# Optimization experiments

Measured on AMD Instinct MI355X. Metric: run time of the kernel, lower is better.

Reference implementation:

```python
import jax, jax.numpy as jnp
import numpy as np

B, N, CIN = 4, 8192, 256
H, D = 8, 64            # n_heads, head_n_channels
INNER = H * D           # 512
COUT = 256
EPS = 1e-5              # torch InstanceNorm1d default eps


def setup_inputs() -> dict:
    key = jax.random.key(0)
    ks = jax.random.split(key, 8)
    s = 1.0 / np.sqrt(CIN)
    return {
        "u_x": jax.random.normal(ks[0], (B, N, CIN), dtype=jnp.float32),
        "pos_x": jax.random.uniform(ks[1], (B, N, 2), dtype=jnp.float32),
        # torch nn.Linear weights have shape (out_features, in_features)
        "Wq": jax.random.normal(ks[2], (INNER, CIN), dtype=jnp.float32) * s,
        "Wk": jax.random.normal(ks[3], (INNER, CIN), dtype=jnp.float32) * s,
        "Wv": jax.random.normal(ks[4], (INNER, CIN), dtype=jnp.float32) * s,
        "Wo": jax.random.normal(ks[5], (COUT, INNER), dtype=jnp.float32) * (1.0 / np.sqrt(INNER)),
        "bo": jax.random.normal(ks[6], (COUT,), dtype=jnp.float32) * 0.01,
    }


def _heads(x, W):
    # x: [B,N,CIN] @ W.T -> [B,N,H*D] -> [B,H,N,D]
    y = jnp.einsum("bnc,ec->bne", x, W)
    return y.reshape(x.shape[0], x.shape[1], H, D).transpose(0, 2, 1, 3)


def _inorm(u):
    # Matches torch: InstanceNorm1d applied to (B*H, N, D) normalizes over the
    # LAST dim (D) per (batch, head, grid point), biased variance, no affine.
    mean = jnp.mean(u, axis=-1, keepdims=True)
    var = jnp.mean(jnp.square(u - mean), axis=-1, keepdims=True)
    return (u - mean) / jnp.sqrt(var + EPS)


def reference(u_x, pos_x, Wq, Wk, Wv, Wo, bo):
    batch, n = u_x.shape[0], u_x.shape[1]
    q = _heads(u_x, Wq)          # [B,H,N,D]
    k = _inorm(_heads(u_x, Wk))  # u_y = u_x (self-attention path)
    v = _inorm(_heads(u_x, Wv))
    # associative path: (K^T V) then Q; uniform weights = 1/N
    dots = jnp.einsum("bhnd,bhne->bhde", k, v)   # [B,H,D,D]
    u = jnp.einsum("bhnd,bhde->bhne", q, dots) / n
    u = u.transpose(0, 2, 1, 3).reshape(batch, n, INNER)
    return jnp.einsum("bne,oe->bno", u, Wo) + bo
```

## Files before the change

kernel.cpp:

```cpp
#include <hip/hip_runtime.h>


#define B_    4
#define N_    8192
#define CIN_  256
#define H_    8
#define D_    64
#define INNER_ 512
#define COUT_ 256
#define EPS_  1e-5f

typedef unsigned short ushort_t;
typedef unsigned int   uint_t;
typedef __attribute__((ext_vector_type(8))) short short8;
typedef __attribute__((ext_vector_type(4))) float f32x4;

__device__ __forceinline__ void split_bf16(float x, ushort_t& hi, ushort_t& lo) {
  const uint_t u = __float_as_uint(x);
  const uint_t hr = (u + 0x8000u) & 0xffff0000u;
  hi = (ushort_t)(hr >> 16);
  const float l = x - __uint_as_float(hr);
  lo = (ushort_t)((__float_as_uint(l) + 0x8000u) >> 16);
}

__device__ __forceinline__ void cvt8(float4 x, float4 y, uint4& uh, uint4& ul) {
  const float v[8] = {x.x, x.y, x.z, x.w, y.x, y.y, y.z, y.w};
  ushort_t h[8], l[8];
#pragma unroll
  for (int j = 0; j < 8; j++) split_bf16(v[j], h[j], l[j]);
  uh = make_uint4(h[0] | ((uint_t)h[1] << 16), h[2] | ((uint_t)h[3] << 16),
                  h[4] | ((uint_t)h[5] << 16), h[6] | ((uint_t)h[7] << 16));
  ul = make_uint4(l[0] | ((uint_t)l[1] << 16), l[2] | ((uint_t)l[3] << 16),
                  l[4] | ((uint_t)l[5] << 16), l[6] | ((uint_t)l[7] << 16));
}

#define MFMA(A, Bv, C) __builtin_amdgcn_mfma_f32_16x16x32_bf16((A), (Bv), (C), 0, 0, 0)


__global__ __launch_bounds__(256) void prep_ux_kernel(
    const float* __restrict__ u_x, ushort_t* __restrict__ uxH,
    ushort_t* __restrict__ uxL)
{
  const int w = threadIdx.x >> 6, lane = threadIdx.x & 63;
  const uint_t tile = blockIdx.x * 4 + w;
  const uint_t kt = tile & 7, ntg = tile >> 3;
  const uint_t r = lane & 15, qv = lane >> 4;
  const size_t src = ((size_t)ntg * 16 + r) * 256 + kt * 32 + qv * 8;
  const float4 x = *(const float4*)(u_x + src);
  const float4 y = *(const float4*)(u_x + src + 4);
  uint4 uh, ul;
  cvt8(x, y, uh, ul);
  const size_t dst = (size_t)tile * 512 + (size_t)lane * 8;
  *(uint4*)(uxH + dst) = uh;
  *(uint4*)(uxL + dst) = ul;
}

__global__ __launch_bounds__(256) void prep_w_kernel(
    const float* __restrict__ Wk, const float* __restrict__ Wv,
    ushort_t* __restrict__ WkvH, ushort_t* __restrict__ WkvL)
{
  const uint_t tid = blockIdx.x * 256 + threadIdx.x;
  const uint_t rr = tid >> 5;
  const uint_t c0 = (tid & 31) * 8;
  const float* src = (rr < 512) ? (Wk + (size_t)rr * CIN_ + c0)
                                : (Wv + (size_t)(rr - 512) * CIN_ + c0);
  const float4 x = *(const float4*)(src);
  const float4 y = *(const float4*)(src + 4);
  uint4 uh, ul;
  cvt8(x, y, uh, ul);
  const uint_t kt = c0 >> 5, qq = (c0 >> 3) & 3;
  const uint_t lanei = (rr & 15) | (qq << 4);
  const size_t dst = (((size_t)(rr >> 4) * 8 + kt) * 64 + lanei) * 8;
  *(uint4*)(WkvH + dst) = uh;
  *(uint4*)(WkvL + dst) = ul;
}

__global__ __launch_bounds__(256, 2) void kv_dots_kernel(
    const ushort_t* __restrict__ uxH, const ushort_t* __restrict__ uxL,
    const ushort_t* __restrict__ WkvH, const ushort_t* __restrict__ WkvL,
    float* __restrict__ dots)
{
  __shared__ __align__(16) char smem[32768];
  ushort_t* KtH = (ushort_t*)(smem);
  ushort_t* KtL = (ushort_t*)(smem + 8192);
  ushort_t* VtH = (ushort_t*)(smem + 16384);
  ushort_t* VtL = (ushort_t*)(smem + 24576);

  const int t = threadIdx.x;
  const int chunk = blockIdx.x, h = blockIdx.y, b = blockIdx.z;
  const int lane = t & 63, wave = t >> 6;
  const int q = lane >> 4, r = lane & 15;
  const int m0 = (wave >> 1) * 64;
  const int dstripe = 16 * wave;
  const size_t laneoff = (size_t)lane * 8;

  const int rtB0 = ((wave & 1) ? 32 : 0) + h * 4;

  f32x4 dacc[4];
#pragma unroll
  for (int j = 0; j < 4; j++) dacc[j] = (f32x4)0.f;

  for (int mt = 0; mt < 2; mt++) {
    const int nt0 = chunk * 16 + mt * 8 + (m0 >> 4);

    f32x4 acc[4][4];
#pragma unroll
    for (int i = 0; i < 4; i++)
#pragma unroll
      for (int j = 0; j < 4; j++) acc[i][j] = (f32x4)0.f;

    for (int kc = 0; kc < 8; kc++) {
      short8 ahf[4], alf[4];
#pragma unroll
      for (int mi = 0; mi < 4; mi++) {
        const size_t toff =
            (((size_t)b * 512 + nt0 + mi) * 8 + kc) * 512 + laneoff;
        ahf[mi] = *(const short8*)(uxH + toff);
        alf[mi] = *(const short8*)(uxL + toff);
      }
#pragma unroll
      for (int nj = 0; nj < 4; nj++) {
        const size_t boff = ((size_t)(rtB0 + nj) * 8 + kc) * 512 + laneoff;
        const short8 bhv = *(const short8*)(WkvH + boff);
        const short8 blv = *(const short8*)(WkvL + boff);
#pragma unroll
        for (int mi = 0; mi < 4; mi++) {
          acc[mi][nj] = MFMA(ahf[mi], bhv, acc[mi][nj]);
          acc[mi][nj] = MFMA(alf[mi], bhv, acc[mi][nj]);
          acc[mi][nj] = MFMA(ahf[mi], blv, acc[mi][nj]);
        }
      }
    }

    float mean[4][4], inv[4][4];
#pragma unroll
    for (int mi = 0; mi < 4; mi++)
#pragma unroll
      for (int reg = 0; reg < 4; reg++) {
        float rs = 0.f, rq = 0.f;
#pragma unroll
        for (int nj = 0; nj < 4; nj++) {
          const float v = acc[mi][nj][reg];
          rs += v;
          rq = fmaf(v, v, rq);
        }
#pragma unroll
        for (int msk = 1; msk < 16; msk <<= 1) {
          rs += __shfl_xor(rs, msk, 64);
          rq += __shfl_xor(rq, msk, 64);
        }
        const float m = rs * (1.f / 64.f);
        const float var = fmaxf(rq * (1.f / 64.f) - m * m, 0.f);
        mean[mi][reg] = m;
        inv[mi][reg] = rsqrtf(var + EPS_);
      }
#pragma unroll
    for (int mi = 0; mi < 4; mi++)
#pragma unroll
      for (int nj = 0; nj < 4; nj++)
#pragma unroll
        for (int reg = 0; reg < 4; reg++)
          acc[mi][nj][reg] = (acc[mi][nj][reg] - mean[mi][reg]) * inv[mi][reg];

    for (int p = 0; p < 2; p++) {
      if ((wave >> 1) == p) {
        ushort_t* Hd = (wave & 1) ? VtH : KtH;
        ushort_t* Ld = (wave & 1) ? VtL : KtL;
#pragma unroll
        for (int nj = 0; nj < 4; nj++) {
          const int d = 16 * nj + r;
#pragma unroll
          for (int mi = 0; mi < 4; mi++) {
            ushort_t hh[4], ll[4];
#pragma unroll
            for (int reg = 0; reg < 4; reg++)
              split_bf16(acc[mi][nj][reg], hh[reg], ll[reg]);
            uint2 ph, pl;
            ph.x = hh[0] | ((uint_t)hh[1] << 16);
            ph.y = hh[2] | ((uint_t)hh[3] << 16);
            pl.x = ll[0] | ((uint_t)ll[1] << 16);
            pl.y = ll[2] | ((uint_t)ll[3] << 16);
            const int bw = ((4 * mi + q) ^ ((d & 7) << 1)) * 4;
            *(uint2*)&Hd[d * 64 + bw] = ph;
            *(uint2*)&Ld[d * 64 + bw] = pl;
          }
        }
      }
      __syncthreads();
#pragma unroll
      for (int ks = 0; ks < 2; ks++) {
        const int ra = dstripe + r;
        const int ca = ((ks * 4 + q) ^ (ra & 7)) * 8;
        const short8 aH = *(const short8*)&KtH[ra * 64 + ca];
        const short8 aL = *(const short8*)&KtL[ra * 64 + ca];
#pragma unroll
        for (int ej = 0; ej < 4; ej++) {
          const int rb = 16 * ej + r;
          const int cb = ((ks * 4 + q) ^ (rb & 7)) * 8;
          const short8 bH = *(const short8*)&VtH[rb * 64 + cb];
          const short8 bL = *(const short8*)&VtL[rb * 64 + cb];
          dacc[ej] = MFMA(aH, bH, dacc[ej]);
          dacc[ej] = MFMA(aL, bH, dacc[ej]);
          dacc[ej] = MFMA(aH, bL, dacc[ej]);
        }
      }
      __syncthreads();
    }
  }

  float* dg = dots + ((size_t)(b * H_ + h)) * 4096;
#pragma unroll
  for (int ej = 0; ej < 4; ej++)
#pragma unroll
    for (int reg = 0; reg < 4; reg++)
      atomicAdd(&dg[(dstripe + 4 * q + reg) * 64 + 16 * ej + r], dacc[ej][reg]);
}

__global__ __launch_bounds__(256) void s_kernel(
    const float* __restrict__ dots, const float* __restrict__ Wo,
    float* __restrict__ S)
{
  const int blk = blockIdx.x;
  const int b = blk >> 9, hd = blk & 511, h = hd >> 6;
  __shared__ float drow[64];
  const int t = threadIdx.x;
  if (t < 64) drow[t] = dots[((size_t)(b * H_ + h)) * 4096 + (hd & 63) * 64 + t];
  __syncthreads();
  const float* wp = Wo + (size_t)t * INNER_ + h * 64;
  float acc = 0.f;
#pragma unroll
  for (int e = 0; e < 64; e += 4) {
    const float4 w = *(const float4*)(wp + e);
    acc = fmaf(drow[e + 0], w.x, acc);
    acc = fmaf(drow[e + 1], w.y, acc);
    acc = fmaf(drow[e + 2], w.z, acc);
    acc = fmaf(drow[e + 3], w.w, acc);
  }
  S[((size_t)(b * INNER_) + hd) * COUT_ + t] = acc;
}

__global__ __launch_bounds__(256) void mb_part_kernel(
    const float* __restrict__ Wq, const float* __restrict__ S,
    float* __restrict__ Mbp)
{
  __shared__ __align__(16) float wql[128][16];
  const int c0 = blockIdx.x * 16, b = blockIdx.y, s = blockIdx.z;
  const int t = threadIdx.x;
#pragma unroll
  for (int i = 0; i < 8; i++) {
    const int idx = i * 256 + t;
    wql[idx >> 4][idx & 15] = Wq[(size_t)(s * 128 + (idx >> 4)) * CIN_ + c0 + (idx & 15)];
  }
  __syncthreads();
  float acc[16];
#pragma unroll
  for (int cp = 0; cp < 16; cp++) acc[cp] = 0.f;
  const float* sp = S + ((size_t)(b * INNER_) + s * 128) * COUT_ + t;
  for (int hd = 0; hd < 128; hd++) {
    const float sv = sp[(size_t)hd * COUT_];
#pragma unroll
    for (int g = 0; g < 4; g++) {
      const float4 w = *(const float4*)&wql[hd][g * 4];
      acc[g * 4 + 0] = fmaf(w.x, sv, acc[g * 4 + 0]);
      acc[g * 4 + 1] = fmaf(w.y, sv, acc[g * 4 + 1]);
      acc[g * 4 + 2] = fmaf(w.z, sv, acc[g * 4 + 2]);
      acc[g * 4 + 3] = fmaf(w.w, sv, acc[g * 4 + 3]);
    }
  }
#pragma unroll
  for (int cp = 0; cp < 16; cp++)
    Mbp[(((size_t)s * 4 + b) * CIN_ + c0 + cp) * COUT_ + t] = acc[cp];
}

__global__ __launch_bounds__(256) void mb_merge_kernel(
    const float* __restrict__ Mbp, ushort_t* __restrict__ MbtH,
    ushort_t* __restrict__ MbtL)
{
  const int c0 = blockIdx.x * 16, b = blockIdx.y;
  const int o = threadIdx.x;
#pragma unroll
  for (int cp = 0; cp < 16; cp++) {
    const int c = c0 + cp;
    float v = 0.f;
#pragma unroll
    for (int s = 0; s < 4; s++)
      v += Mbp[(((size_t)s * 4 + b) * CIN_ + c) * COUT_ + o];
    v *= (1.0f / N_);
    ushort_t hi, lo;
    split_bf16(v, hi, lo);
    const uint_t kt = c >> 5, qq = (c >> 3) & 3;
    const uint_t lanei = (o & 15) | (qq << 4);
    const size_t off =
        ((((size_t)b * 16 + (o >> 4)) * 8 + kt) * 64 + lanei) * 8 + (c & 7);
    MbtH[off] = hi;
    MbtL[off] = lo;
  }
}

__global__ __launch_bounds__(256, 2) void out_kernel(
    const ushort_t* __restrict__ uxH, const ushort_t* __restrict__ uxL,
    const ushort_t* __restrict__ MbtH, const ushort_t* __restrict__ MbtL,
    const float* __restrict__ bo, float* __restrict__ out)
{
  const int t = threadIdx.x;
  const int r0 = blockIdx.x * 128, o0 = blockIdx.y * 128, b = blockIdx.z;
  const int lane = t & 63, wave = t >> 6;
  const int q = lane >> 4, r = lane & 15;
  const int m0 = (wave >> 1) * 64, n0 = (wave & 1) * 64;
  const size_t laneoff = (size_t)lane * 8;

  const int nt0 = (r0 + m0) >> 4;
  const int ot0 = (o0 + n0) >> 4;

  f32x4 acc[4][4];
#pragma unroll
  for (int i = 0; i < 4; i++)
#pragma unroll
    for (int j = 0; j < 4; j++) acc[i][j] = (f32x4)0.f;

  for (int kc = 0; kc < 8; kc++) {
    short8 ahf[4], alf[4];
#pragma unroll
    for (int mi = 0; mi < 4; mi++) {
      const size_t toff =
          (((size_t)b * 512 + nt0 + mi) * 8 + kc) * 512 + laneoff;
      ahf[mi] = *(const short8*)(uxH + toff);
      alf[mi] = *(const short8*)(uxL + toff);
    }
#pragma unroll
    for (int nj = 0; nj < 4; nj++) {
      const size_t boff =
          (((size_t)b * 16 + ot0 + nj) * 8 + kc) * 512 + laneoff;
      const short8 bhv = *(const short8*)(MbtH + boff);
      const short8 blv = *(const short8*)(MbtL + boff);
#pragma unroll
      for (int mi = 0; mi < 4; mi++) {
        acc[mi][nj] = MFMA(ahf[mi], bhv, acc[mi][nj]);
        acc[mi][nj] = MFMA(alf[mi], bhv, acc[mi][nj]);
        acc[mi][nj] = MFMA(ahf[mi], blv, acc[mi][nj]);
      }
    }
  }

  float bov[4];
#pragma unroll
  for (int nj = 0; nj < 4; nj++) bov[nj] = bo[o0 + n0 + 16 * nj + r];
#pragma unroll
  for (int mi = 0; mi < 4; mi++)
#pragma unroll
    for (int nj = 0; nj < 4; nj++) {
      const f32x4 v = acc[mi][nj];
#pragma unroll
      for (int reg = 0; reg < 4; reg++) {
        const int row = r0 + m0 + 16 * mi + q * 4 + reg;
        out[((size_t)(b * N_) + row) * COUT_ + o0 + n0 + 16 * nj + r] =
            v[reg] + bov[nj];
      }
    }
}

extern "C" void kernel_launch(void* const* d_in, const int* in_sizes, int n_in,
                              void* d_out, int out_size, void* d_ws, size_t ws_size,
                              hipStream_t stream) {
  const float* u_x = (const float*)d_in[0];
  const float* Wq = (const float*)d_in[2];
  const float* Wk = (const float*)d_in[3];
  const float* Wv = (const float*)d_in[4];
  const float* Wo = (const float*)d_in[5];
  const float* bo = (const float*)d_in[6];
  float* out = (float*)d_out;

  ushort_t* uxH  = (ushort_t*)d_ws;
  ushort_t* uxL  = uxH + 8388608;
  ushort_t* WkvH = uxL + 8388608;
  ushort_t* WkvL = WkvH + 262144;
  ushort_t* MbtH = WkvL + 262144;
  ushort_t* MbtL = MbtH + 262144;
  float* dots = (float*)(MbtL + 262144);
  float* S    = dots + 131072;
  float* Mbp  = S + 524288;

  prep_ux_kernel<<<4096, 256, 0, stream>>>(u_x, uxH, uxL);
  prep_w_kernel<<<128, 256, 0, stream>>>(Wk, Wv, WkvH, WkvL);
  hipMemsetAsync(dots, 0, 131072 * sizeof(float), stream);
  kv_dots_kernel<<<dim3(32, 8, 4), 256, 0, stream>>>(uxH, uxL, WkvH, WkvL, dots);
  s_kernel<<<2048, 256, 0, stream>>>(dots, Wo, S);
  mb_part_kernel<<<dim3(16, 4, 4), 256, 0, stream>>>(Wq, S, Mbp);
  mb_merge_kernel<<<dim3(16, 4), 256, 0, stream>>>(Mbp, MbtH, MbtL);
  out_kernel<<<dim3(64, 2, 4), 256, 0, stream>>>(uxH, uxL, MbtH, MbtL, bo, out);
}
```

Before: 231.2 us.

## Widen KV LDS staging to process both row halves per barrier pair, add setprio

```diff
diff --git a/kernel.cpp b/kernel.cpp
--- a/kernel.cpp
+++ b/kernel.cpp
@@ -80,11 +80,11 @@
     const ushort_t* __restrict__ WkvH, const ushort_t* __restrict__ WkvL,
     float* __restrict__ dots)
 {
-  __shared__ __align__(16) char smem[32768];
+  __shared__ __align__(16) char smem[65536];
   ushort_t* KtH = (ushort_t*)(smem);
-  ushort_t* KtL = (ushort_t*)(smem + 8192);
-  ushort_t* VtH = (ushort_t*)(smem + 16384);
-  ushort_t* VtL = (ushort_t*)(smem + 24576);
+  ushort_t* KtL = (ushort_t*)(smem + 16384);
+  ushort_t* VtH = (ushort_t*)(smem + 32768);
+  ushort_t* VtL = (ushort_t*)(smem + 49152);
 
   const int t = threadIdx.x;
   const int chunk = blockIdx.x, h = blockIdx.y, b = blockIdx.z;
@@ -109,6 +109,7 @@
 #pragma unroll
       for (int j = 0; j < 4; j++) acc[i][j] = (f32x4)0.f;
 
+#pragma unroll 2
     for (int kc = 0; kc < 8; kc++) {
       short8 ahf[4], alf[4];
 #pragma unroll
@@ -118,6 +119,7 @@
         ahf[mi] = *(const short8*)(uxH + toff);
         alf[mi] = *(const short8*)(uxL + toff);
       }
+      __builtin_amdgcn_s_setprio(1);
 #pragma unroll
       for (int nj = 0; nj < 4; nj++) {
         const size_t boff = ((size_t)(rtB0 + nj) * 8 + kc) * 512 + laneoff;
@@ -130,6 +132,7 @@
           acc[mi][nj] = MFMA(ahf[mi], blv, acc[mi][nj]);
         }
       }
+      __builtin_amdgcn_s_setprio(0);
     }
 
     float mean[4][4], inv[4][4];
@@ -162,50 +165,52 @@
         for (int reg = 0; reg < 4; reg++)
           acc[mi][nj][reg] = (acc[mi][nj][reg] - mean[mi][reg]) * inv[mi][reg];
 
-    for (int p = 0; p < 2; p++) {
-      if ((wave >> 1) == p) {
-        ushort_t* Hd = (wave & 1) ? VtH : KtH;
-        ushort_t* Ld = (wave & 1) ? VtL : KtL;
-#pragma unroll
-        for (int nj = 0; nj < 4; nj++) {
-          const int d = 16 * nj + r;
-#pragma unroll
-          for (int mi = 0; mi < 4; mi++) {
-            ushort_t hh[4], ll[4];
-#pragma unroll
-            for (int reg = 0; reg < 4; reg++)
-              split_bf16(acc[mi][nj][reg], hh[reg], ll[reg]);
-            uint2 ph, pl;
-            ph.x = hh[0] | ((uint_t)hh[1] << 16);
-            ph.y = hh[2] | ((uint_t)hh[3] << 16);
-            pl.x = ll[0] | ((uint_t)ll[1] << 16);
-            pl.y = ll[2] | ((uint_t)ll[3] << 16);
-            const int bw = ((4 * mi + q) ^ ((d & 7) << 1)) * 4;
-            *(uint2*)&Hd[d * 64 + bw] = ph;
-            *(uint2*)&Ld[d * 64 + bw] = pl;
-          }
+    __syncthreads();
+    {
+      ushort_t* Hd = (wave & 1) ? VtH : KtH;
+      ushort_t* Ld = (wave & 1) ? VtL : KtL;
+      const int so16 = (wave >> 1) * 16;
+#pragma unroll
+      for (int nj = 0; nj < 4; nj++) {
+        const int d = 16 * nj + r;
+#pragma unroll
+        for (int mi = 0; mi < 4; mi++) {
+          ushort_t hh[4], ll[4];
+#pragma unroll
+          for (int reg = 0; reg < 4; reg++)
+            split_bf16(acc[mi][nj][reg], hh[reg], ll[reg]);
+          uint2 ph, pl;
+          ph.x = hh[0] | ((uint_t)hh[1] << 16);
+          ph.y = hh[2] | ((uint_t)hh[3] << 16);
+          pl.x = ll[0] | ((uint_t)ll[1] << 16);
+          pl.y = ll[2] | ((uint_t)ll[3] << 16);
+          const int wb = so16 | ((4 * mi + q) ^ ((d & 7) << 1));
+          *(uint2*)&Hd[d * 128 + wb * 4] = ph;
+          *(uint2*)&Ld[d * 128 + wb * 4] = pl;
         }
       }
-      __syncthreads();
-#pragma unroll
-      for (int ks = 0; ks < 2; ks++) {
-        const int ra = dstripe + r;
-        const int ca = ((ks * 4 + q) ^ (ra & 7)) * 8;
-        const short8 aH = *(const short8*)&KtH[ra * 64 + ca];
-        const short8 aL = *(const short8*)&KtL[ra * 64 + ca];
-#pragma unroll
-        for (int ej = 0; ej < 4; ej++) {
-          const int rb = 16 * ej + r;
-          const int cb = ((ks * 4 + q) ^ (rb & 7)) * 8;
-          const short8 bH = *(const short8*)&VtH[rb * 64 + cb];
-          const short8 bL = *(const short8*)&VtL[rb * 64 + cb];
-          dacc[ej] = MFMA(aH, bH, dacc[ej]);
-          dacc[ej] = MFMA(aL, bH, dacc[ej]);
-          dacc[ej] = MFMA(aH, bL, dacc[ej]);
-        }
-      }
-      __syncthreads();
-    }
+    }
+    __syncthreads();
+    __builtin_amdgcn_s_setprio(1);
+#pragma unroll
+    for (int ks = 0; ks < 4; ks++) {
+      const int ra = dstripe + r;
+      const int cb = ks * 4 + q;
+      const int sbA = (cb & 8) | ((cb & 7) ^ (ra & 7));
+      const short8 aH = *(const short8*)&KtH[ra * 128 + sbA * 8];
+      const short8 aL = *(const short8*)&KtL[ra * 128 + sbA * 8];
+#pragma unroll
+      for (int ej = 0; ej < 4; ej++) {
+        const int rb = 16 * ej + r;
+        const int sbB = (cb & 8) | ((cb & 7) ^ (rb & 7));
+        const short8 bH = *(const short8*)&VtH[rb * 128 + sbB * 8];
+        const short8 bL = *(const short8*)&VtL[rb * 128 + sbB * 8];
+        dacc[ej] = MFMA(aH, bH, dacc[ej]);
+        dacc[ej] = MFMA(aL, bH, dacc[ej]);
+        dacc[ej] = MFMA(aH, bL, dacc[ej]);
+      }
+    }
+    __builtin_amdgcn_s_setprio(0);
   }
 
   float* dg = dots + ((size_t)(b * H_ + h)) * 4096;
@@ -318,6 +323,7 @@
 #pragma unroll
     for (int j = 0; j < 4; j++) acc[i][j] = (f32x4)0.f;
 
+#pragma unroll 2
   for (int kc = 0; kc < 8; kc++) {
     short8 ahf[4], alf[4];
 #pragma unroll
@@ -327,6 +333,7 @@
       ahf[mi] = *(const short8*)(uxH + toff);
       alf[mi] = *(const short8*)(uxL + toff);
     }
+    __builtin_amdgcn_s_setprio(1);
 #pragma unroll
     for (int nj = 0; nj < 4; nj++) {
       const size_t boff =
@@ -340,6 +347,7 @@
         acc[mi][nj] = MFMA(ahf[mi], blv, acc[mi][nj]);
       }
     }
+    __builtin_amdgcn_s_setprio(0);
   }
 
   float bov[4];
```

Result: no change. 231.2 us (-0.0%).

## Stage GEMM operands through double-buffered LDS via direct global-to-LDS loads

Applied to the files above, without the earlier changes.

```diff
diff --git a/kernel.cpp b/kernel.cpp
--- a/kernel.cpp
+++ b/kernel.cpp
@@ -36,6 +36,12 @@
 
 #define MFMA(A, Bv, C) __builtin_amdgcn_mfma_f32_16x16x32_bf16((A), (Bv), (C), 0, 0, 0)
 
+__device__ __forceinline__ void gl_lds16(const ushort_t* g, char* l) {
+  __builtin_amdgcn_global_load_lds(
+      (const __attribute__((address_space(1))) void*)(const void*)g,
+      (__attribute__((address_space(3))) void*)(void*)l, 16, 0, 0);
+}
+
 
 __global__ __launch_bounds__(256) void prep_ux_kernel(
     const float* __restrict__ u_x, ushort_t* __restrict__ uxH,
@@ -43,9 +49,9 @@
 {
   const int w = threadIdx.x >> 6, lane = threadIdx.x & 63;
   const uint_t tile = blockIdx.x * 4 + w;
-  const uint_t kt = tile & 7, ntg = tile >> 3;
+  const uint_t b = tile >> 12, kt = (tile >> 9) & 7, nt = tile & 511;
   const uint_t r = lane & 15, qv = lane >> 4;
-  const size_t src = ((size_t)ntg * 16 + r) * 256 + kt * 32 + qv * 8;
+  const size_t src = ((size_t)(b * 8192 + nt * 16 + r)) * 256 + kt * 32 + qv * 8;
   const float4 x = *(const float4*)(u_x + src);
   const float4 y = *(const float4*)(u_x + src + 4);
   uint4 uh, ul;
@@ -70,7 +76,7 @@
   cvt8(x, y, uh, ul);
   const uint_t kt = c0 >> 5, qq = (c0 >> 3) & 3;
   const uint_t lanei = (rr & 15) | (qq << 4);
-  const size_t dst = (((size_t)(rr >> 4) * 8 + kt) * 64 + lanei) * 8;
+  const size_t dst = (((size_t)kt * 64 + (rr >> 4)) * 64 + lanei) * 8;
   *(uint4*)(WkvH + dst) = uh;
   *(uint4*)(WkvL + dst) = ul;
 }
@@ -80,7 +86,7 @@
     const ushort_t* __restrict__ WkvH, const ushort_t* __restrict__ WkvL,
     float* __restrict__ dots)
 {
-  __shared__ __align__(16) char smem[32768];
+  __shared__ __align__(16) char smem[65536];
   ushort_t* KtH = (ushort_t*)(smem);
   ushort_t* KtL = (ushort_t*)(smem + 8192);
   ushort_t* VtH = (ushort_t*)(smem + 16384);
@@ -90,18 +96,26 @@
   const int chunk = blockIdx.x, h = blockIdx.y, b = blockIdx.z;
   const int lane = t & 63, wave = t >> 6;
   const int q = lane >> 4, r = lane & 15;
-  const int m0 = (wave >> 1) * 64;
   const int dstripe = 16 * wave;
-  const size_t laneoff = (size_t)lane * 8;
-
-  const int rtB0 = ((wave & 1) ? 32 : 0) + h * 4;
+  const size_t lane8 = (size_t)lane * 8;
+  const int laneB = lane * 16;
+
+  const int aSlot = (wave >> 1) * 4;
+  const int bSlot = 16 + (wave & 1) * 4;
+
+  const size_t kcA = 512 * 512, kcB = 64 * 512;
 
   f32x4 dacc[4];
 #pragma unroll
   for (int j = 0; j < 4; j++) dacc[j] = (f32x4)0.f;
 
   for (int mt = 0; mt < 2; mt++) {
-    const int nt0 = chunk * 16 + mt * 8 + (m0 >> 4);
+    const int ntB = chunk * 16 + mt * 8;
+
+    const ushort_t* pA = ((wave == 0) ? uxH : uxL) +
+                         ((size_t)(b * 8) * 512 + ntB) * 512 + lane8;
+    const ushort_t* pKV = ((wave == 2) ? WkvH : WkvL) +
+                          (size_t)(h * 4) * 512 + lane8;
 
     f32x4 acc[4][4];
 #pragma unroll
@@ -109,20 +123,51 @@
 #pragma unroll
       for (int j = 0; j < 4; j++) acc[i][j] = (f32x4)0.f;
 
+    if (wave < 2) {
+#pragma unroll
+      for (int j = 0; j < 8; j++)
+        gl_lds16(pA + j * 512, smem + (wave * 8 + j) * 1024);
+    } else {
+#pragma unroll
+      for (int j = 0; j < 4; j++) {
+        gl_lds16(pKV + j * 512, smem + (16 + (wave - 2) * 8 + j) * 1024);
+        gl_lds16(pKV + 16384 + j * 512,
+                 smem + (16 + (wave - 2) * 8 + 4 + j) * 1024);
+      }
+    }
+    pA += kcA;
+    pKV += kcB;
+    __syncthreads();
+
     for (int kc = 0; kc < 8; kc++) {
+      if (kc < 7) {
+        char* d = smem + (((kc + 1) & 1)) * 32768;
+        if (wave < 2) {
+#pragma unroll
+          for (int j = 0; j < 8; j++)
+            gl_lds16(pA + j * 512, d + (wave * 8 + j) * 1024);
+        } else {
+#pragma unroll
+          for (int j = 0; j < 4; j++) {
+            gl_lds16(pKV + j * 512, d + (16 + (wave - 2) * 8 + j) * 1024);
+            gl_lds16(pKV + 16384 + j * 512,
+                     d + (16 + (wave - 2) * 8 + 4 + j) * 1024);
+          }
+        }
+        pA += kcA;
+        pKV += kcB;
+      }
+      const char* sb = smem + (kc & 1) * 32768;
       short8 ahf[4], alf[4];
 #pragma unroll
       for (int mi = 0; mi < 4; mi++) {
-        const size_t toff =
-            (((size_t)b * 512 + nt0 + mi) * 8 + kc) * 512 + laneoff;
-        ahf[mi] = *(const short8*)(uxH + toff);
-        alf[mi] = *(const short8*)(uxL + toff);
+        ahf[mi] = *(const short8*)(sb + (aSlot + mi) * 1024 + laneB);
+        alf[mi] = *(const short8*)(sb + (8 + aSlot + mi) * 1024 + laneB);
       }
 #pragma unroll
       for (int nj = 0; nj < 4; nj++) {
-        const size_t boff = ((size_t)(rtB0 + nj) * 8 + kc) * 512 + laneoff;
-        const short8 bhv = *(const short8*)(WkvH + boff);
-        const short8 blv = *(const short8*)(WkvL + boff);
+        const short8 bhv = *(const short8*)(sb + (bSlot + nj) * 1024 + laneB);
+        const short8 blv = *(const short8*)(sb + (8 + bSlot + nj) * 1024 + laneB);
 #pragma unroll
         for (int mi = 0; mi < 4; mi++) {
           acc[mi][nj] = MFMA(ahf[mi], bhv, acc[mi][nj]);
@@ -130,6 +175,7 @@
           acc[mi][nj] = MFMA(ahf[mi], blv, acc[mi][nj]);
         }
       }
+      __syncthreads();
     }
 
     float mean[4][4], inv[4][4];
@@ -291,7 +337,7 @@
     const uint_t kt = c >> 5, qq = (c >> 3) & 3;
     const uint_t lanei = (o & 15) | (qq << 4);
     const size_t off =
-        ((((size_t)b * 16 + (o >> 4)) * 8 + kt) * 64 + lanei) * 8 + (c & 7);
+        ((((size_t)(b * 8 + kt)) * 16 + (o >> 4)) * 64 + lanei) * 8 + (c & 7);
     MbtH[off] = hi;
     MbtL[off] = lo;
   }
@@ -302,15 +348,24 @@
     const ushort_t* __restrict__ MbtH, const ushort_t* __restrict__ MbtL,
     const float* __restrict__ bo, float* __restrict__ out)
 {
+  __shared__ __align__(16) char smem[65536];
   const int t = threadIdx.x;
   const int r0 = blockIdx.x * 128, o0 = blockIdx.y * 128, b = blockIdx.z;
   const int lane = t & 63, wave = t >> 6;
   const int q = lane >> 4, r = lane & 15;
   const int m0 = (wave >> 1) * 64, n0 = (wave & 1) * 64;
-  const size_t laneoff = (size_t)lane * 8;
-
-  const int nt0 = (r0 + m0) >> 4;
-  const int ot0 = (o0 + n0) >> 4;
+  const size_t lane8 = (size_t)lane * 8;
+  const int laneB = lane * 16;
+
+  const int ntB = r0 >> 4, otB = o0 >> 4;
+  const int aSlot = (wave >> 1) * 4;
+  const int bSlot = 16 + (wave & 1) * 4;
+  const size_t kcA = 512 * 512, kcB = 16 * 512;
+
+  const ushort_t* pA = ((wave == 0) ? uxH : uxL) +
+                       ((size_t)(b * 8) * 512 + ntB) * 512 + lane8;
+  const ushort_t* pB = ((wave == 2) ? MbtH : MbtL) +
+                       ((size_t)(b * 8) * 16 + otB) * 512 + lane8;
 
   f32x4 acc[4][4];
 #pragma unroll
@@ -318,21 +373,45 @@
 #pragma unroll
     for (int j = 0; j < 4; j++) acc[i][j] = (f32x4)0.f;
 
+  if (wave < 2) {
+#pragma unroll
+    for (int j = 0; j < 8; j++)
+      gl_lds16(pA + j * 512, smem + (wave * 8 + j) * 1024);
+  } else {
+#pragma unroll
+    for (int j = 0; j < 8; j++)
+      gl_lds16(pB + j * 512, smem + (16 + (wave - 2) * 8 + j) * 1024);
+  }
+  pA += kcA;
+  pB += kcB;
+  __syncthreads();
+
   for (int kc = 0; kc < 8; kc++) {
+    if (kc < 7) {
+      char* d = smem + (((kc + 1) & 1)) * 32768;
+      if (wave < 2) {
+#pragma unroll
+        for (int j = 0; j < 8; j++)
+          gl_lds16(pA + j * 512, d + (wave * 8 + j) * 1024);
+      } else {
+#pragma unroll
+        for (int j = 0; j < 8; j++)
+          gl_lds16(pB + j * 512, d + (16 + (wave - 2) * 8 + j) * 1024);
+      }
+      pA += kcA;
+      pB += kcB;
+    }
+    const char* sb = smem + (kc & 1) * 32768;
     short8 ahf[4], alf[4];
 #pragma unroll
     for (int mi = 0; mi < 4; mi++) {
-      const size_t toff =
-          (((size_t)b * 512 + nt0 + mi) * 8 + kc) * 512 + laneoff;
-      ahf[mi] = *(const short8*)(uxH + toff);
-      alf[mi] = *(const short8*)(uxL + toff);
+      ahf[mi] = *(const short8*)(sb + (aSlot + mi) * 1024 + laneB);
+      alf[mi] = *(const short8*)(sb + (8 + aSlot + mi) * 1024 + laneB);
     }
 #pragma unroll
     for (int nj = 0; nj < 4; nj++) {
-      const size_t boff =
-          (((size_t)b * 16 + ot0 + nj) * 8 + kc) * 512 + laneoff;
-      const short8 bhv = *(const short8*)(MbtH + boff);
-      const short8 blv = *(const short8*)(MbtL + boff);
+      const short8 bhv = *(const short8*)(sb + (bSlot + nj) * 1024 + laneB);
+      const short8 blv = *(const short8*)(sb + (8 + bSlot + nj) * 1024 + laneB);
 #pragma unroll
       for (int mi = 0; mi < 4; mi++) {
         acc[mi][nj] = MFMA(ahf[mi], bhv, acc[mi][nj]);
@@ -340,6 +419,7 @@
         acc[mi][nj] = MFMA(ahf[mi], blv, acc[mi][nj]);
       }
     }
+    __syncthreads();
   }
 
   float bov[4];
```

New measurement: 260.3 us. +12.6%, slower.
